# Performance work log

Measured on AMD Instinct MI355X. Metric: run time of the kernel, lower is better.

The kernel has to match this reference:

```python
import jax, jax.numpy as jnp
import numpy as np

T, B, H, V, L = 512, 8, 256, 32000, 3
THRESH = 1.0

# Heaviside spike with ATan surrogate gradient (snntorch default, alpha=2)
@jax.custom_vjp
def spike(u):
    return (u > 0).astype(u.dtype)

def _spike_fwd(u):
    return (u > 0).astype(u.dtype), u

def _spike_bwd(u, g):
    return (g / (1.0 + (jnp.pi * u) ** 2),)

spike.defvjp(_spike_fwd, _spike_bwd)


def leaky_scan(cur, beta):
    """mem[t] = beta * mem[t-1] + cur[t]; cur: (T,B,H), beta: (H,). No reset -> associative."""
    def step(mem, c):
        mem = beta * mem + c
        return mem, mem
    _, mems = jax.lax.scan(step, jnp.zeros(cur.shape[1:], cur.dtype), cur)
    return mems  # (T,B,H)


def setup_inputs() -> dict:
    key = jax.random.key(0)
    ks = jax.random.split(key, 10)
    s = 1.0 / np.sqrt(H)
    return {
        "tokens": jax.random.randint(ks[0], (T, B), 0, V),
        "token_emb": jax.random.normal(ks[1], (V, H), dtype=jnp.float32) * 0.02,
        "pos_emb": jax.random.normal(ks[2], (T, H), dtype=jnp.float32) * 0.02,
        "Wq": jax.random.normal(ks[3], (L, H, H), dtype=jnp.float32) * s,
        "bq": jnp.zeros((L, H), dtype=jnp.float32),
        "beta": jax.random.uniform(ks[4], (L, H), minval=0.5, maxval=0.95),
        "Wfc": jax.random.normal(ks[5], (L, H, H), dtype=jnp.float32) * s,
        "bfc": jnp.zeros((L, H), dtype=jnp.float32),
        "Wout": jax.random.normal(ks[6], (H, V), dtype=jnp.float32) * s,
        "bout": jnp.zeros((V,), dtype=jnp.float32),
    }


def reference(tokens, token_emb, pos_emb, Wq, bq, beta, Wfc, bfc, Wout, bout):
    # embed: (T,B,H) + broadcast positional (T,1,H)
    h = token_emb[tokens] + pos_emb[:, None, :]
    for l in range(L):  # small fixed layer count
        cur = jnp.einsum('tbh,hd->tbd', h, Wq[l]) + bq[l]   # q-projection
        mem = leaky_scan(cur, beta[l])                       # leaky integrate, no reset
        spk = spike(mem - THRESH)                            # heaviside spikes
        h = jax.nn.relu(jnp.einsum('tbh,hd->tbd', spk, Wfc[l]) + bfc[l])
    logits = jnp.einsum('tbh,hv->tbv', h, Wout) + bout       # (T,B,V)
    return logits
```

## Files before the change

kernel.cpp:

```cpp
#include <hip/hip_runtime.h>
#include <hip/hip_bf16.h>
#include <cstddef>

constexpr int T_ = 512;
constexpr int B_ = 8;
constexpr int H_ = 256;
constexpr int V_ = 32000;
constexpr int L_ = 3;
constexpr int M_ = T_ * B_;

typedef __attribute__((ext_vector_type(8))) short short8;
typedef __attribute__((ext_vector_type(4))) float floatx4;

__device__ __forceinline__ unsigned short f2bf(float f) {
    unsigned u = __float_as_uint(f);
    u += 0x7fffu + ((u >> 16) & 1u);
    return (unsigned short)(u >> 16);
}

__device__ __forceinline__ void gl_lds16(const void* g, void* l) {
    __builtin_amdgcn_global_load_lds((__attribute__((address_space(1))) void*)g,
                                     (__attribute__((address_space(3))) void*)l,
                                     16, 0, 0);
}

__global__ __launch_bounds__(256) void embed_kernel(
    const int* __restrict__ tokens, const float* __restrict__ temb,
    const float* __restrict__ pemb, unsigned short* __restrict__ hb)
{
    const int idx = blockIdx.x * 256 + threadIdx.x;
    const int h4 = idx & (H_ / 4 - 1);
    const int tb = idx >> 6;
    const int b  = tb & (B_ - 1);
    const int t  = tb >> 3;
    const int tok = tokens[t * B_ + b];
    const float4 e = *(const float4*)&temb[(size_t)tok * H_ + h4 * 4];
    const float4 p = *(const float4*)&pemb[(size_t)t * H_ + h4 * 4];
    ushort4 r;
    r.x = f2bf(e.x + p.x); r.y = f2bf(e.y + p.y);
    r.z = f2bf(e.z + p.z); r.w = f2bf(e.w + p.w);
    *(ushort4*)&hb[(size_t)idx * 4] = r;
}

constexpr int CH_ = 32;
constexpr int NT_ = T_ / CH_;
constexpr int TS_ = B_ * H_;

__global__ __launch_bounds__(256) void scan_local_kernel(
    const float* __restrict__ cur, const float* __restrict__ beta_l,
    float* __restrict__ mloc)
{
    const int c = blockIdx.x, b = blockIdx.y, h = threadIdx.x;
    const float bt = beta_l[h];
    const size_t off = ((size_t)(c * CH_) * B_ + b) * H_ + h;
    const float* p = cur + off;
    float* q = mloc + off;
    float mem = 0.0f;
    #pragma unroll
    for (int tt = 0; tt < CH_; ++tt) {
        mem = fmaf(bt, mem, p[(size_t)tt * TS_]);
        q[(size_t)tt * TS_] = mem;
    }
}

__global__ __launch_bounds__(256) void scan_apply_kernel(
    const float* __restrict__ mloc, const float* __restrict__ beta_l,
    unsigned short* __restrict__ spk)
{
    const int c = blockIdx.x, b = blockIdx.y, h = threadIdx.x;
    const float bt = beta_l[h];
    float b32 = bt;
    #pragma unroll
    for (int i = 0; i < 5; ++i) b32 *= b32;
    float carry = 0.0f;
    for (int j = 0; j < c; ++j)
        carry = fmaf(b32, carry,
                     mloc[((size_t)(j * CH_ + CH_ - 1) * B_ + b) * H_ + h]);
    const size_t off = ((size_t)(c * CH_) * B_ + b) * H_ + h;
    const float* p = mloc + off;
    unsigned short* q = spk + off;
    float pw = bt;
    #pragma unroll
    for (int tt = 0; tt < CH_; ++tt) {
        const float mem = fmaf(pw, carry, p[(size_t)tt * TS_]);
        pw *= bt;
        q[(size_t)tt * TS_] = (mem > 1.0f) ? (unsigned short)0x3F80u
                                           : (unsigned short)0u;
    }
}

__global__ __launch_bounds__(256) void transpose_small_kernel(
    const float* __restrict__ Wq, const float* __restrict__ Wfc,
    unsigned short* __restrict__ WT)
{
    __shared__ float t[64][65];
    const int z = blockIdx.z;
    const float* src = (z < 3) ? Wq + (size_t)z * H_ * H_
                               : Wfc + (size_t)(z - 3) * H_ * H_;
    unsigned short* dst = WT + (size_t)z * H_ * H_;
    const int n0 = blockIdx.x * 64, k0 = blockIdx.y * 64;
    const int x = threadIdx.x & 63, y = threadIdx.x >> 6;
    #pragma unroll
    for (int i = 0; i < 16; ++i)
        t[y + 4 * i][x] = src[(size_t)(k0 + y + 4 * i) * H_ + n0 + x];
    __syncthreads();
    #pragma unroll
    for (int i = 0; i < 16; ++i)
        dst[(size_t)(n0 + y + 4 * i) * H_ + k0 + x] = f2bf(t[x][y + 4 * i]);
}

__global__ __launch_bounds__(256) void transpose_wout_kernel(
    const float* __restrict__ W, unsigned short* __restrict__ Wt)
{
    __shared__ float t[64][65];
    const int n0 = blockIdx.x * 64;
    const int k0 = blockIdx.y * 64;
    const int x = threadIdx.x & 63, y = threadIdx.x >> 6;
    #pragma unroll
    for (int i = 0; i < 16; ++i)
        t[y + 4 * i][x] = W[(size_t)(k0 + y + 4 * i) * V_ + n0 + x];
    __syncthreads();
    #pragma unroll
    for (int i = 0; i < 16; ++i)
        Wt[(size_t)(n0 + y + 4 * i) * H_ + k0 + x] = f2bf(t[x][y + 4 * i]);
}


__global__ __launch_bounds__(256) void gemm_mfma_out(
    const unsigned short* __restrict__ A,
    const unsigned short* __restrict__ Bt,
    const float* __restrict__ bias,
    float* __restrict__ C)
{
    constexpr int K = H_, N = V_;
    __shared__ __align__(16) short lA[1024][8];
    __shared__ __align__(16) short lB[1024][8];

    const int tid = threadIdx.x;
    const int lane = tid & 63, wave = tid >> 6;
    const int wm = wave >> 1, wn = wave & 1;
    const int l15 = lane & 15, quad = lane >> 4;
    const int m0 = blockIdx.x * 128;
    const int n0 = blockIdx.y * 128;

    floatx4 acc[4][4] = {};

    for (int k0 = 0; k0 < K; k0 += 64) {
        #pragma unroll
        for (int j = 0; j < 4; ++j) {
            const int base = (wave * 4 + j) * 64;
            const int s = base + lane;
            const int row = s >> 3;
            const int oct = (s & 7) ^ (row & 7);
            gl_lds16(A  + (size_t)(m0 + row) * K + k0 + oct * 8, &lA[base][0]);
            gl_lds16(Bt + (size_t)(n0 + row) * K + k0 + oct * 8, &lB[base][0]);
        }
        __syncthreads();

        #pragma unroll
        for (int t = 0; t < 2; ++t) {
            short8 af[4], bf[4];
            #pragma unroll
            for (int f = 0; f < 4; ++f) {
                const int ra = wm * 64 + f * 16 + l15;
                const int rb = wn * 64 + f * 16 + l15;
                af[f] = *(const short8*)&lA[ra * 8 + ((4 * t + quad) ^ (ra & 7))][0];
                bf[f] = *(const short8*)&lB[rb * 8 + ((4 * t + quad) ^ (rb & 7))][0];
            }
            #pragma unroll
            for (int i = 0; i < 4; ++i)
                #pragma unroll
                for (int j2 = 0; j2 < 4; ++j2)
                    acc[i][j2] = __builtin_amdgcn_mfma_f32_16x16x32_bf16(
                        af[i], bf[j2], acc[i][j2], 0, 0, 0);
        }
        __syncthreads();
    }

    #pragma unroll
    for (int j2 = 0; j2 < 4; ++j2) {
        const int col = n0 + wn * 64 + j2 * 16 + l15;
        const float bv = bias[col];
        #pragma unroll
        for (int i = 0; i < 4; ++i) {
            const int rbase = m0 + wm * 64 + i * 16 + quad * 4;
            #pragma unroll
            for (int r = 0; r < 4; ++r)
                C[(size_t)(rbase + r) * N + col] = acc[i][j2][r] + bv;
        }
    }
}

template <int RELU, int OUT_BF16>
__global__ __launch_bounds__(256) void gemm_mfma_layer(
    const unsigned short* __restrict__ A,
    const unsigned short* __restrict__ Bt,
    const float* __restrict__ bias,
    float* __restrict__ Cf, unsigned short* __restrict__ Cb)
{
    constexpr int K = H_, N = H_;
    __shared__ __align__(16) short lA[1024][8];
    __shared__ __align__(16) short lB[512][8];

    const int tid = threadIdx.x;
    const int lane = tid & 63, wave = tid >> 6;
    const int wm = wave >> 1, wn = wave & 1;
    const int l15 = lane & 15, quad = lane >> 4;
    const int m0 = blockIdx.x * 128;
    const int n0 = blockIdx.y * 64;

    floatx4 acc[4][2] = {};

    for (int k0 = 0; k0 < K; k0 += 64) {
        #pragma unroll
        for (int j = 0; j < 4; ++j) {
            const int base = (wave * 4 + j) * 64;
            const int s = base + lane;
            const int row = s >> 3;
            const int oct = (s & 7) ^ (row & 7);
            gl_lds16(A + (size_t)(m0 + row) * K + k0 + oct * 8, &lA[base][0]);
        }
        #pragma unroll
        for (int j = 0; j < 2; ++j) {
            const int base = (wave * 2 + j) * 64;
            const int s = base + lane;
            const int row = s >> 3;
            const int oct = (s & 7) ^ (row & 7);
            gl_lds16(Bt + (size_t)(n0 + row) * K + k0 + oct * 8, &lB[base][0]);
        }
        __syncthreads();

        #pragma unroll
        for (int t = 0; t < 2; ++t) {
            short8 af[4], bf[2];
            #pragma unroll
            for (int f = 0; f < 4; ++f) {
                const int ra = wm * 64 + f * 16 + l15;
                af[f] = *(const short8*)&lA[ra * 8 + ((4 * t + quad) ^ (ra & 7))][0];
            }
            #pragma unroll
            for (int f = 0; f < 2; ++f) {
                const int rb = wn * 32 + f * 16 + l15;
                bf[f] = *(const short8*)&lB[rb * 8 + ((4 * t + quad) ^ (rb & 7))][0];
            }
            #pragma unroll
            for (int i = 0; i < 4; ++i)
                #pragma unroll
                for (int j2 = 0; j2 < 2; ++j2)
                    acc[i][j2] = __builtin_amdgcn_mfma_f32_16x16x32_bf16(
                        af[i], bf[j2], acc[i][j2], 0, 0, 0);
        }
        __syncthreads();
    }

    #pragma unroll
    for (int j2 = 0; j2 < 2; ++j2) {
        const int col = n0 + wn * 32 + j2 * 16 + l15;
        const float bv = bias[col];
        #pragma unroll
        for (int i = 0; i < 4; ++i) {
            const int rbase = m0 + wm * 64 + i * 16 + quad * 4;
            #pragma unroll
            for (int r = 0; r < 4; ++r) {
                float v = acc[i][j2][r] + bv;
                if (RELU) v = fmaxf(v, 0.0f);
                if (OUT_BF16)
                    Cb[(size_t)(rbase + r) * N + col] = f2bf(v);
                else
                    Cf[(size_t)(rbase + r) * N + col] = v;
            }
        }
    }
}

extern "C" void kernel_launch(void* const* d_in, const int* in_sizes, int n_in,
                              void* d_out, int out_size, void* d_ws, size_t ws_size,
                              hipStream_t stream)
{
    const int*   tokens = (const int*)  d_in[0];
    const float* temb   = (const float*)d_in[1];
    const float* pemb   = (const float*)d_in[2];
    const float* Wq     = (const float*)d_in[3];
    const float* bq     = (const float*)d_in[4];
    const float* beta   = (const float*)d_in[5];
    const float* Wfc    = (const float*)d_in[6];
    const float* bfc    = (const float*)d_in[7];
    const float* Wout   = (const float*)d_in[8];
    const float* bout   = (const float*)d_in[9];
    float* out = (float*)d_out;

    unsigned short* h_bf  = (unsigned short*)d_ws;
    unsigned short* spk   = h_bf + (size_t)M_ * H_;
    unsigned short* WT    = spk + (size_t)M_ * H_;
    unsigned short* WoutT = WT + (size_t)2 * L_ * H_ * H_;
    float*          cur   = (float*)(WoutT + (size_t)V_ * H_);
    float*          mloc  = cur + (size_t)M_ * H_;

    transpose_small_kernel<<<dim3(4, 4, 6), 256, 0, stream>>>(Wq, Wfc, WT);
    transpose_wout_kernel<<<dim3(V_ / 64, H_ / 64), 256, 0, stream>>>(Wout, WoutT);

    embed_kernel<<<(M_ * H_ / 4) / 256, 256, 0, stream>>>(tokens, temb, pemb, h_bf);

    for (int l = 0; l < L_; ++l) {
        const unsigned short* WqT  = WT + (size_t)l * H_ * H_;
        const unsigned short* WfcT = WT + (size_t)(L_ + l) * H_ * H_;
        gemm_mfma_layer<0, 0><<<dim3(M_ / 128, H_ / 64), 256, 0, stream>>>(
            h_bf, WqT, bq + (size_t)l * H_, cur, nullptr);
        scan_local_kernel<<<dim3(NT_, B_), 256, 0, stream>>>(
            cur, beta + (size_t)l * H_, mloc);
        scan_apply_kernel<<<dim3(NT_, B_), 256, 0, stream>>>(
            mloc, beta + (size_t)l * H_, spk);
        gemm_mfma_layer<1, 1><<<dim3(M_ / 128, H_ / 64), 256, 0, stream>>>(
            spk, WfcT, bfc + (size_t)l * H_, nullptr, h_bf);
    }

    gemm_mfma_out<<<dim3(M_ / 128, V_ / 128), 256, 0, stream>>>(
        h_bf, WoutT, bout, out);
}
```

Measured before the change: 738.2 us.

## Restructure output GEMM to keep full-K Wout tile in LDS, stream activations

The vocab projection GEMM now loads a whole 128xK slice of transposed Wout into LDS once per block. Each wave then loops over 64-row M strips, reading activation fragments directly from global memory with the full K resident. MFMA operands are swapped so each lane writes four consecutive output columns as a float4 nontemporal store, replacing scattered scalar stores. The goal is to cut per-k-step barriers and global-to-LDS traffic and to make the large fp32 logits write more efficient, at the cost of uncached direct global loads of A and high register use from 32 accumulators.

```diff
diff --git a/kernel.cpp b/kernel.cpp
--- a/kernel.cpp
+++ b/kernel.cpp
@@ -125,68 +125,69 @@
         Wt[(size_t)(n0 + y + 4 * i) * H_ + k0 + x] = f2bf(t[x][y + 4 * i]);
 }
 
-
-__global__ __launch_bounds__(256) void gemm_mfma_out(
+__global__ __launch_bounds__(256, 2) void gemm_mfma_out(
     const unsigned short* __restrict__ A,
     const unsigned short* __restrict__ Bt,
     const float* __restrict__ bias,
     float* __restrict__ C)
 {
     constexpr int K = H_, N = V_;
-    __shared__ __align__(16) short lA[1024][8];
-    __shared__ __align__(16) short lB[1024][8];
+    __shared__ __align__(16) short lB[4096][8];
 
     const int tid = threadIdx.x;
     const int lane = tid & 63, wave = tid >> 6;
-    const int wm = wave >> 1, wn = wave & 1;
     const int l15 = lane & 15, quad = lane >> 4;
-    const int m0 = blockIdx.x * 128;
+    const int mh0 = blockIdx.x * 2048;
     const int n0 = blockIdx.y * 128;
 
-    floatx4 acc[4][4] = {};
-
-    for (int k0 = 0; k0 < K; k0 += 64) {
-        #pragma unroll
-        for (int j = 0; j < 4; ++j) {
-            const int base = (wave * 4 + j) * 64;
-            const int s = base + lane;
-            const int row = s >> 3;
-            const int oct = (s & 7) ^ (row & 7);
-            gl_lds16(A  + (size_t)(m0 + row) * K + k0 + oct * 8, &lA[base][0]);
-            gl_lds16(Bt + (size_t)(n0 + row) * K + k0 + oct * 8, &lB[base][0]);
-        }
-        __syncthreads();
-
-        #pragma unroll
-        for (int t = 0; t < 2; ++t) {
-            short8 af[4], bf[4];
-            #pragma unroll
-            for (int f = 0; f < 4; ++f) {
-                const int ra = wm * 64 + f * 16 + l15;
-                const int rb = wn * 64 + f * 16 + l15;
-                af[f] = *(const short8*)&lA[ra * 8 + ((4 * t + quad) ^ (ra & 7))][0];
-                bf[f] = *(const short8*)&lB[rb * 8 + ((4 * t + quad) ^ (rb & 7))][0];
-            }
-            #pragma unroll
-            for (int i = 0; i < 4; ++i)
+    #pragma unroll
+    for (int g = 0; g < 16; ++g) {
+        const int base = (wave * 16 + g) * 64;
+        const int s = base + lane;
+        const int row = s >> 5;
+        const int oct = (s & 24) | ((s & 7) ^ (row & 7));
+        gl_lds16(Bt + (size_t)(n0 + row) * K + oct * 8, &lB[base][0]);
+    }
+    __syncthreads();
+
+    for (int ms = wave; ms < 32; ms += 4) {
+        const int m0 = mh0 + ms * 64;
+        floatx4 acc[8][4] = {};
+        #pragma unroll
+        for (int ks = 0; ks < 8; ++ks) {
+            short8 hf[4], wf[8];
+            #pragma unroll
+            for (int j = 0; j < 4; ++j)
+                hf[j] = *(const short8*)&A[(size_t)(m0 + j * 16 + l15) * K
+                                           + ks * 32 + quad * 8];
+            #pragma unroll
+            for (int i = 0; i < 8; ++i) {
+                const int rb = i * 16 + l15;
+                const int o = ks * 4 + quad;
+                const int os = (o & 24) | ((o & 7) ^ (rb & 7));
+                wf[i] = *(const short8*)&lB[rb * 32 + os][0];
+            }
+            #pragma unroll
+            for (int i = 0; i < 8; ++i)
                 #pragma unroll
-                for (int j2 = 0; j2 < 4; ++j2)
-                    acc[i][j2] = __builtin_amdgcn_mfma_f32_16x16x32_bf16(
-                        af[i], bf[j2], acc[i][j2], 0, 0, 0);
-        }
-        __syncthreads();
-    }
-
-    #pragma unroll
-    for (int j2 = 0; j2 < 4; ++j2) {
-        const int col = n0 + wn * 64 + j2 * 16 + l15;
-        const float bv = bias[col];
-        #pragma unroll
-        for (int i = 0; i < 4; ++i) {
-            const int rbase = m0 + wm * 64 + i * 16 + quad * 4;
-            #pragma unroll
-            for (int r = 0; r < 4; ++r)
-                C[(size_t)(rbase + r) * N + col] = acc[i][j2][r] + bv;
+                for (int j = 0; j < 4; ++j)
+                    acc[i][j] = __builtin_amdgcn_mfma_f32_16x16x32_bf16(
+                        wf[i], hf[j], acc[i][j], 0, 0, 0);
+        }
+        #pragma unroll
+        for (int i = 0; i < 8; ++i) {
+            const int n = n0 + i * 16 + quad * 4;
+            const float4 bv = *(const float4*)&bias[n];
+            #pragma unroll
+            for (int j = 0; j < 4; ++j) {
+                const int m = m0 + j * 16 + l15;
+                floatx4 v;
+                v[0] = acc[i][j][0] + bv.x;
+                v[1] = acc[i][j][1] + bv.y;
+                v[2] = acc[i][j][2] + bv.z;
+                v[3] = acc[i][j][3] + bv.w;
+                __builtin_nontemporal_store(v, (floatx4*)&C[(size_t)m * N + n]);
+            }
         }
     }
 }
@@ -314,6 +315,6 @@
             spk, WfcT, bfc + (size_t)l * H_, nullptr, h_bf);
     }
 
-    gemm_mfma_out<<<dim3(M_ / 128, V_ / 128), 256, 0, stream>>>(
+    gemm_mfma_out<<<dim3(M_ / 2048, V_ / 128), 256, 0, stream>>>(
         h_bf, WoutT, bout, out);
 }
```

After: 804.5 us. 1.09x slower.
